# Kernel tuning notes

Hardware: AMD Instinct MI355X
Metric: run time of the kernel (lower is better)

Reference implementation:

```python
import jax, jax.numpy as jnp
import numpy as np

DIM = 256
NUM_HEAD = 8
HEAD_DIM = DIM // NUM_HEAD
SCALE = HEAD_DIM ** -0.5


def setup_inputs() -> dict:
    key = jax.random.key(0)
    ks = jax.random.split(key, 8)
    B, NQ, NK = 8, 512, 4096
    state = jax.random.normal(ks[0], (B, NQ, DIM), dtype=jnp.float32)
    pointcloud = jax.random.normal(ks[1], (B, NK, DIM), dtype=jnp.float32)
    s = 0.02
    Wq = jax.random.normal(ks[2], (DIM, DIM), dtype=jnp.float32) * s
    bq = jnp.zeros((DIM,), dtype=jnp.float32)
    Wkv = jax.random.normal(ks[3], (DIM, 2 * DIM), dtype=jnp.float32) * s
    bkv = jnp.zeros((2 * DIM,), dtype=jnp.float32)
    Wo = jax.random.normal(ks[4], (DIM, DIM), dtype=jnp.float32) * s
    bo = jnp.zeros((DIM,), dtype=jnp.float32)
    return {"state": state, "pointcloud": pointcloud, "Wq": Wq, "bq": bq,
            "Wkv": Wkv, "bkv": bkv, "Wo": Wo, "bo": bo}


def reference(state, pointcloud, Wq, bq, Wkv, bkv, Wo, bo):
    # q: [b, nq, dim]; kv: [b, nk, 2*dim]
    q = state @ Wq + bq
    kv = pointcloud @ Wkv + bkv
    k, v = jnp.split(kv, 2, axis=-1)

    def split_heads(x):
        b, n, _ = x.shape
        return x.reshape(b, n, NUM_HEAD, HEAD_DIM).transpose(0, 2, 1, 3)  # b h n d

    q, k, v = split_heads(q), split_heads(k), split_heads(v)
    attn = jnp.einsum('bhqd,bhkd->bhqk', q, k) * SCALE
    attn = jax.nn.softmax(attn, axis=-1)
    out = jnp.einsum('bhqk,bhkd->bhqd', attn, v)
    b, h, nq, d = out.shape
    out = out.transpose(0, 2, 1, 3).reshape(b, nq, h * d)
    return out @ Wo + bo
```

## Files before the change

### kernel.cpp

```cpp
#include <hip/hip_runtime.h>

typedef unsigned short u16;
typedef unsigned int   u32;
typedef __bf16 bf16x8 __attribute__((ext_vector_type(8)));
typedef float  f32x4  __attribute__((ext_vector_type(4)));
typedef float  f32x16 __attribute__((ext_vector_type(16)));
typedef u32    u32x4  __attribute__((ext_vector_type(4)));
typedef u16    u16x8  __attribute__((ext_vector_type(8)));

#define DEVINL __device__ __forceinline__

DEVINL void glds16(const void* g, void* l) {
  __builtin_amdgcn_global_load_lds((const __attribute__((address_space(1))) u32*)g,
                                   (__attribute__((address_space(3))) u32*)l, 16, 0, 0);
}

DEVINL u16 f2bf(float f) {
  u32 u = __builtin_bit_cast(u32, f);
  u32 r = u + 0x7fffu + ((u >> 16) & 1u);
  return (u16)(r >> 16);
}

DEVINL u32 cvtpk(float lo, float hi) {
  u32 r;
  asm("v_cvt_pk_bf16_f32 %0, %1, %2" : "=v"(r) : "v"(lo), "v"(hi));
  return r;
}

DEVINL u16x8 cvt8(f32x4 a, f32x4 b) {
  u32x4 r = {cvtpk(a[0], a[1]), cvtpk(a[2], a[3]), cvtpk(b[0], b[1]), cvtpk(b[2], b[3])};
  return __builtin_bit_cast(u16x8, r);
}

__global__ __launch_bounds__(256) void prep_k(const float* __restrict__ Wq,
                                              const float* __restrict__ Wkv,
                                              const float* __restrict__ Wo,
                                              const float* __restrict__ state,
                                              const float* __restrict__ pc,
                                              u16* __restrict__ WqT, u16* __restrict__ WkvT,
                                              u16* __restrict__ WoT, u16* __restrict__ sb,
                                              u16* __restrict__ pb) {
  int bid = blockIdx.x, tid = threadIdx.x;
  if (bid < 1024) {
    int i = bid * 256 + tid;
    if (i < 65536) {
      int n = i >> 8, k = i & 255;
      WqT[i] = f2bf(Wq[k * 256 + n]);
    } else if (i < 196608) {
      int j = i - 65536; int n = j >> 8, k = j & 255;
      WkvT[j] = f2bf(Wkv[k * 512 + n]);
    } else {
      int j = i - 196608; int n = j >> 8, k = j & 255;
      WoT[j] = f2bf(Wo[k * 256 + n]);
    }
  } else if (bid < 1536) {
    size_t u = (size_t)(bid - 1024) * 256 + tid;
    f32x4 a = *(const f32x4*)(state + u * 8);
    f32x4 b = *(const f32x4*)(state + u * 8 + 4);
    *(u16x8*)(sb + u * 8) = cvt8(a, b);
  } else {
    size_t u = (size_t)(bid - 1536) * 256 + tid;
    f32x4 a = *(const f32x4*)(pc + u * 8);
    f32x4 b = *(const f32x4*)(pc + u * 8 + 4);
    *(u16x8*)(pb + u * 8) = cvt8(a, b);
  }
}

template<int EPI, bool XCDSWZ>
DEVINL void gemm_body(const u16* __restrict__ A, const u16* __restrict__ Bt,
                      const float* __restrict__ bias, void* __restrict__ Cp,
                      void* __restrict__ C2p, u16* As, u16* Bs,
                      int N, int nmt, float scale, int bid, int nblk) {
  const int K = 256;
  int tid = threadIdx.x, lane = tid & 63, w = tid >> 6;
  int g = lane >> 4, ln15 = lane & 15;
  int mt, nt;
  if (XCDSWZ) {
    int u = (bid & 7) * (nblk >> 3) + (bid >> 3);
    mt = u >> 2; nt = u & 3;
  } else {
    mt = bid % nmt; nt = bid / nmt;
  }
  int arow0 = mt * 128, bcol0 = nt * 128;
  int wr = w >> 1, wc = w & 1;
  f32x4 acc[4][4] = {};

  auto stage = [&](int buf, int kt) {
    #pragma unroll
    for (int i = 0; i < 4; ++i) {
      int c = i * 256 + tid; int row = c >> 3, seg = c & 7;
      glds16(A + (size_t)(arow0 + row) * K + kt * 64 + (seg ^ (row & 7)) * 8,
             (char*)As + (size_t)buf * 16384 + (i * 256 + w * 64) * 16);
      glds16(Bt + (size_t)(bcol0 + row) * K + kt * 64 + (seg ^ (row & 7)) * 8,
             (char*)Bs + (size_t)buf * 16384 + (i * 256 + w * 64) * 16);
    }
  };

  stage(0, 0);
  __syncthreads();
  for (int kt = 0; kt < 4; ++kt) {
    int buf = kt & 1;
    if (kt < 3) stage(buf ^ 1, kt + 1);
    const u16* Ab = As + buf * 8192;
    const u16* Bb = Bs + buf * 8192;
    #pragma unroll
    for (int kk = 0; kk < 2; ++kk) {
      bf16x8 af[4], bfr[4];
      #pragma unroll
      for (int mi = 0; mi < 4; ++mi) {
        int row = wr * 64 + mi * 16 + ln15;
        int idx = row * 8 + ((kk * 4 + g) ^ (row & 7));
        af[mi] = __builtin_bit_cast(bf16x8, *(const u32x4*)&Ab[idx * 8]);
      }
      #pragma unroll
      for (int ni = 0; ni < 4; ++ni) {
        int row = wc * 64 + ni * 16 + ln15;
        int idx = row * 8 + ((kk * 4 + g) ^ (row & 7));
        bfr[ni] = __builtin_bit_cast(bf16x8, *(const u32x4*)&Bb[idx * 8]);
      }
      #pragma unroll
      for (int mi = 0; mi < 4; ++mi)
        #pragma unroll
        for (int ni = 0; ni < 4; ++ni)
          acc[mi][ni] = __builtin_amdgcn_mfma_f32_16x16x32_bf16(af[mi], bfr[ni], acc[mi][ni], 0, 0, 0);
    }
    __syncthreads();
  }
  #pragma unroll
  for (int mi = 0; mi < 4; ++mi) {
    #pragma unroll
    for (int ni = 0; ni < 4; ++ni) {
      int col = bcol0 + wc * 64 + ni * 16 + ln15;
      float bv = bias[col];
      #pragma unroll
      for (int r = 0; r < 4; ++r) {
        int row = arow0 + wr * 64 + mi * 16 + g * 4 + r;
        float v = acc[mi][ni][r] + bv;
        if (EPI == 0) {
          ((float*)Cp)[(size_t)row * N + col] = v;
        } else if (EPI == 1) {
          ((u16*)Cp)[(size_t)row * N + col] = f2bf(v * scale);
        } else {
          int b = row >> 12, nk = row & 4095;
          if (col < 256) {
            int h = col >> 5, d = col & 31;
            ((u16*)Cp)[((size_t)((b << 3) + h) * 4096 + nk) * 32 + d] = f2bf(v);
          } else {
            int c2 = col - 256; int h = c2 >> 5, d = c2 & 31;
            ((u16*)C2p)[((size_t)((b << 3) + h) * 4096 + nk) * 32 + d] = f2bf(v);
          }
        }
      }
    }
  }
}

__global__ __launch_bounds__(256) void gemm12_k(const u16* __restrict__ sb,
                                                const u16* __restrict__ pb,
                                                const u16* __restrict__ WqT,
                                                const u16* __restrict__ WkvT,
                                                const float* __restrict__ bq,
                                                const float* __restrict__ bkv,
                                                u16* __restrict__ qbuf, u16* __restrict__ kbuf,
                                                u16* __restrict__ vbuf, float qscl) {
  __shared__ __align__(16) u16 As[2 * 8192];
  __shared__ __align__(16) u16 Bs[2 * 8192];
  int bid = blockIdx.x;
  if (bid < 1024) {
    gemm_body<2, true >(pb, WkvT, bkv, kbuf, vbuf, As, Bs, 512, 256, 1.f, bid, 1024);
  } else {
    gemm_body<1, false>(sb, WqT, bq, qbuf, nullptr, As, Bs, 256, 32, qscl, bid - 1024, 64);
  }
}

__global__ __launch_bounds__(256) void gemm3_k(const u16* __restrict__ ob,
                                               const u16* __restrict__ WoT,
                                               const float* __restrict__ bo,
                                               float* __restrict__ out) {
  __shared__ __align__(16) u16 As[2 * 8192];
  __shared__ __align__(16) u16 Bs[2 * 8192];
  gemm_body<0, false>(ob, WoT, bo, out, nullptr, As, Bs, 256, 32, 1.f, blockIdx.x, 64);
}

__global__ __launch_bounds__(256) void reduce_k(const float* __restrict__ Op,
                                                const float* __restrict__ Dp,
                                                u16* __restrict__ ob) {
  size_t u = (size_t)blockIdx.x * 256 + threadIdx.x;
  int row = (int)(u >> 5), q8 = (int)(u & 31);
  int h = q8 >> 2;
  size_t base = u * 8;
  f32x4 lo = {}, hi = {};
  float dsum = 0.f;
  #pragma unroll
  for (int ss = 0; ss < 4; ++ss) {
    const float* p = Op + (size_t)ss * 1048576;
    lo += *(const f32x4*)(p + base);
    hi += *(const f32x4*)(p + base + 4);
    dsum += Dp[((size_t)ss * 4096 + row) * 8 + h];
  }
  float inv = 1.0f / dsum;
  lo *= inv; hi *= inv;
  *(u16x8*)(ob + base) = cvt8(lo, hi);
}

__global__ __launch_bounds__(256) void attn_k(const u16* __restrict__ qb,
                                              const u16* __restrict__ kb,
                                              const u16* __restrict__ vb,
                                              float* __restrict__ Op,
                                              float* __restrict__ Dp) {
  __shared__ __align__(16) u16 Ks[2][2048];
  __shared__ __align__(16) u16 Vt[2][2048];
  int tid = threadIdx.x, lane = tid & 63, w = tid >> 6;
  int hi = lane >> 5, ln31 = lane & 31;
  int bid = blockIdx.x;
  int qblk = bid >> 8, r2 = bid & 255, bh = r2 >> 2, s = r2 & 3;
  int b = bh >> 3, h = bh & 7;
  const u16* khead = kb + ((size_t)bh * 4096 + s * 1024) * 32;
  const u16* vhead = vb + ((size_t)bh * 4096 + s * 1024) * 32;
  int qrow0 = b * 512 + qblk * 128 + w * 32;

  bf16x8 qf[2];
  #pragma unroll
  for (int ks = 0; ks < 2; ++ks) {
    const u16* src = qb + (size_t)(qrow0 + ln31) * 256 + h * 32 + ks * 16 + hi * 8;
    qf[ks] = __builtin_bit_cast(bf16x8, *(const u32x4*)src);
  }

  f32x16 O = {};
  float den = 0.f;
  int vrow = tid >> 2, vdc = tid & 3;

  auto loadV = [&](int t) -> u32x4 {
    return *(const u32x4*)(vhead + ((size_t)t * 64 + vrow) * 32 + vdc * 8);
  };
  auto stage = [&](int buf, int t, u32x4 vv) {
    glds16(khead + ((size_t)t * 64 + lane) * 32 + w * 8, (char*)&Ks[buf][0] + w * 1024);
    u16x8 us = __builtin_bit_cast(u16x8, vv);
    #pragma unroll
    for (int j = 0; j < 8; ++j) {
      int d = vdc * 8 + j;
      int cs = (vrow >> 3) ^ j ^ (vdc << 1);
      Vt[buf][d * 64 + cs * 8 + (vrow & 7)] = us[j];
    }
  };

  u32x4 vv = loadV(0);
  stage(0, 0, vv);
  vv = loadV(1);
  __syncthreads();

  for (int t = 0; t < 16; ++t) {
    int buf = t & 1;
    if (t + 1 < 16) {
      stage(buf ^ 1, t + 1, vv);
      vv = loadV(t + 2 < 16 ? t + 2 : 15);
    }
    f32x16 sT[2] = {};
    #pragma unroll
    for (int ks = 0; ks < 2; ++ks) {
      #pragma unroll
      for (int mt = 0; mt < 2; ++mt) {
        const u16* ka = &Ks[buf][((ks * 2 + hi) * 64 + mt * 32 + ln31) * 8];
        bf16x8 kf = __builtin_bit_cast(bf16x8, *(const u32x4*)ka);
        sT[mt] = __builtin_amdgcn_mfma_f32_32x32x16_bf16(kf, qf[ks], sT[mt], 0, 0, 0);
      }
    }
    u32 pa[4][4];
    #pragma unroll
    for (int mt = 0; mt < 2; ++mt) {
      float p[16];
      #pragma unroll
      for (int r = 0; r < 16; ++r) p[r] = __builtin_amdgcn_exp2f(sT[mt][r]);
      #pragma unroll
      for (int r = 0; r < 16; ++r) den += p[r];
      u32 pk0[4], pk1[4];
      #pragma unroll
      for (int c = 0; c < 4; ++c) {
        pk0[c] = cvtpk(p[4*c+0], p[4*c+1]);
        pk1[c] = cvtpk(p[4*c+2], p[4*c+3]);
      }
      u32 a0 = pk0[0], b0 = pk0[1];
      asm("v_permlane32_swap_b32 %0, %1" : "+v"(a0), "+v"(b0));
      u32 a1 = pk1[0], b1 = pk1[1];
      asm("v_permlane32_swap_b32 %0, %1" : "+v"(a1), "+v"(b1));
      u32 a2 = pk0[2], b2 = pk0[3];
      asm("v_permlane32_swap_b32 %0, %1" : "+v"(a2), "+v"(b2));
      u32 a3 = pk1[2], b3 = pk1[3];
      asm("v_permlane32_swap_b32 %0, %1" : "+v"(a3), "+v"(b3));
      pa[mt*2+0][0] = a0; pa[mt*2+0][1] = a1; pa[mt*2+0][2] = b0; pa[mt*2+0][3] = b1;
      pa[mt*2+1][0] = a2; pa[mt*2+1][1] = a3; pa[mt*2+1][2] = b2; pa[mt*2+1][3] = b3;
    }
    #pragma unroll
    for (int kst = 0; kst < 4; ++kst) {
      int cs = (kst * 2 + hi) ^ (ln31 & 7) ^ ((ln31 >> 3) << 1);
      const u16* va = &Vt[buf][ln31 * 64 + cs * 8];
      bf16x8 vf = __builtin_bit_cast(bf16x8, *(const u32x4*)va);
      u32x4 paw = {pa[kst][0], pa[kst][1], pa[kst][2], pa[kst][3]};
      O = __builtin_amdgcn_mfma_f32_32x32x16_bf16(__builtin_bit_cast(bf16x8, paw), vf, O, 0, 0, 0);
    }
    __syncthreads();
  }

  den += __shfl_xor(den, 32);
  float* op = Op + (size_t)s * 1048576;
  #pragma unroll
  for (int r = 0; r < 16; ++r) {
    int qr = 8 * (r >> 2) + 4 * hi + (r & 3);
    op[(size_t)(qrow0 + qr) * 256 + h * 32 + ln31] = O[r];
  }
  if (lane < 32) Dp[(size_t)(s * 4096 + qrow0 + ln31) * 8 + h] = den;
}

extern "C" void kernel_launch(void* const* d_in, const int* in_sizes, int n_in,
                              void* d_out, int out_size, void* d_ws, size_t ws_size,
                              hipStream_t stream) {
  const float* state = (const float*)d_in[0];
  const float* pc    = (const float*)d_in[1];
  const float* Wq    = (const float*)d_in[2];
  const float* bq    = (const float*)d_in[3];
  const float* Wkv   = (const float*)d_in[4];
  const float* bkv   = (const float*)d_in[5];
  const float* Wo    = (const float*)d_in[6];
  const float* bo    = (const float*)d_in[7];
  char* ws = (char*)d_ws;
  u16*   WqT  = (u16*)(ws);
  u16*   WkvT = (u16*)(ws + 131072);
  u16*   WoT  = (u16*)(ws + 393216);
  u16*   sb   = (u16*)(ws + 524288);
  u16*   pb   = (u16*)(ws + 2621440);
  u16*   qb   = (u16*)(ws + 19398656);
  u16*   kb   = (u16*)(ws + 21495808);
  u16*   vb   = (u16*)(ws + 38273024);
  u16*   ob   = (u16*)(ws + 55050240);
  float* Op   = (float*)(ws + 57147392);
  float* Dp   = (float*)(ws + 73924608);

  prep_k<<<5632, 256, 0, stream>>>(Wq, Wkv, Wo, state, pc, WqT, WkvT, WoT, sb, pb);
  const float QSCL = 0.17677669529663687f * 1.4426950408889634f;
  gemm12_k<<<1088, 256, 0, stream>>>(sb, pb, WqT, WkvT, bq, bkv, qb, kb, vb, QSCL);
  attn_k<<<1024, 256, 0, stream>>>(qb, kb, vb, Op, Dp);
  reduce_k<<<512, 256, 0, stream>>>(Op, Dp, ob);
  gemm3_k<<<64, 256, 0, stream>>>(ob, WoT, bo, (float*)d_out);
}
```

Before: 156.8 us.

## Double attention key split to 8 and tile weight transpose via LDS

Attention now splits each head's 4096 keys into 8 chunks instead of 4, doubling the grid to 2048 blocks and halving the per-block key loop, with the reduce kernel summing 8 partials. This targets occupancy and tail effects on a GPU with many CUs. The cost is twice the partial output traffic (the fp32 Op buffer doubles and Dp moves to make room). Separately, the weight transpose-and-convert now uses 64x64 shared-memory tiles with coalesced vector loads and stores instead of strided scalar reads.

```diff
diff --git a/kernel.cpp b/kernel.cpp
--- a/kernel.cpp
+++ b/kernel.cpp
@@ -40,26 +40,37 @@
                                               u16* __restrict__ WqT, u16* __restrict__ WkvT,
                                               u16* __restrict__ WoT, u16* __restrict__ sb,
                                               u16* __restrict__ pb) {
+  __shared__ float Lt[64][65];
   int bid = blockIdx.x, tid = threadIdx.x;
-  if (bid < 1024) {
-    int i = bid * 256 + tid;
-    if (i < 65536) {
-      int n = i >> 8, k = i & 255;
-      WqT[i] = f2bf(Wq[k * 256 + n]);
-    } else if (i < 196608) {
-      int j = i - 65536; int n = j >> 8, k = j & 255;
-      WkvT[j] = f2bf(Wkv[k * 512 + n]);
-    } else {
-      int j = i - 196608; int n = j >> 8, k = j & 255;
-      WoT[j] = f2bf(Wo[k * 256 + n]);
-    }
-  } else if (bid < 1536) {
-    size_t u = (size_t)(bid - 1024) * 256 + tid;
+  if (bid < 64) {
+    const float* W; u16* Wt; int Nw, t;
+    if (bid < 16)      { W = Wq;  Wt = WqT;  Nw = 256; t = bid; }
+    else if (bid < 48) { W = Wkv; Wt = WkvT; Nw = 512; t = bid - 16; }
+    else               { W = Wo;  Wt = WoT;  Nw = 256; t = bid - 48; }
+    int kt0 = (t & 3) * 64, nt0 = (t >> 2) * 64;
+    #pragma unroll
+    for (int i = 0; i < 4; ++i) {
+      int idx = i * 256 + tid;
+      int r = idx >> 4, col = (idx & 15) * 4;
+      f32x4 v = *(const f32x4*)(W + (size_t)(kt0 + r) * Nw + nt0 + col);
+      Lt[r][col] = v[0]; Lt[r][col + 1] = v[1]; Lt[r][col + 2] = v[2]; Lt[r][col + 3] = v[3];
+    }
+    __syncthreads();
+    #pragma unroll
+    for (int j = 0; j < 2; ++j) {
+      int idx = j * 256 + tid;
+      int n = idx >> 3, kc = (idx & 7) * 8;
+      f32x4 a = {Lt[kc + 0][n], Lt[kc + 1][n], Lt[kc + 2][n], Lt[kc + 3][n]};
+      f32x4 b = {Lt[kc + 4][n], Lt[kc + 5][n], Lt[kc + 6][n], Lt[kc + 7][n]};
+      *(u16x8*)(Wt + (size_t)(nt0 + n) * 256 + kt0 + kc) = cvt8(a, b);
+    }
+  } else if (bid < 576) {
+    size_t u = (size_t)(bid - 64) * 256 + tid;
     f32x4 a = *(const f32x4*)(state + u * 8);
     f32x4 b = *(const f32x4*)(state + u * 8 + 4);
     *(u16x8*)(sb + u * 8) = cvt8(a, b);
   } else {
-    size_t u = (size_t)(bid - 1536) * 256 + tid;
+    size_t u = (size_t)(bid - 576) * 256 + tid;
     f32x4 a = *(const f32x4*)(pc + u * 8);
     f32x4 b = *(const f32x4*)(pc + u * 8 + 4);
     *(u16x8*)(pb + u * 8) = cvt8(a, b);
@@ -192,7 +203,7 @@
   f32x4 lo = {}, hi = {};
   float dsum = 0.f;
   #pragma unroll
-  for (int ss = 0; ss < 4; ++ss) {
+  for (int ss = 0; ss < 8; ++ss) {
     const float* p = Op + (size_t)ss * 1048576;
     lo += *(const f32x4*)(p + base);
     hi += *(const f32x4*)(p + base + 4);
@@ -213,10 +224,10 @@
   int tid = threadIdx.x, lane = tid & 63, w = tid >> 6;
   int hi = lane >> 5, ln31 = lane & 31;
   int bid = blockIdx.x;
-  int qblk = bid >> 8, r2 = bid & 255, bh = r2 >> 2, s = r2 & 3;
+  int qblk = bid >> 9, r2 = bid & 511, bh = r2 >> 3, s = r2 & 7;
   int b = bh >> 3, h = bh & 7;
-  const u16* khead = kb + ((size_t)bh * 4096 + s * 1024) * 32;
-  const u16* vhead = vb + ((size_t)bh * 4096 + s * 1024) * 32;
+  const u16* khead = kb + ((size_t)bh * 4096 + s * 512) * 32;
+  const u16* vhead = vb + ((size_t)bh * 4096 + s * 512) * 32;
   int qrow0 = b * 512 + qblk * 128 + w * 32;
 
   bf16x8 qf[2];
@@ -249,11 +260,11 @@
   vv = loadV(1);
   __syncthreads();
 
-  for (int t = 0; t < 16; ++t) {
+  for (int t = 0; t < 8; ++t) {
     int buf = t & 1;
-    if (t + 1 < 16) {
+    if (t + 1 < 8) {
       stage(buf ^ 1, t + 1, vv);
-      vv = loadV(t + 2 < 16 ? t + 2 : 15);
+      vv = loadV(t + 2 < 8 ? t + 2 : 7);
     }
     f32x16 sT[2] = {};
     #pragma unroll
@@ -333,12 +344,12 @@
   u16*   vb   = (u16*)(ws + 38273024);
   u16*   ob   = (u16*)(ws + 55050240);
   float* Op   = (float*)(ws + 57147392);
-  float* Dp   = (float*)(ws + 73924608);
-
-  prep_k<<<5632, 256, 0, stream>>>(Wq, Wkv, Wo, state, pc, WqT, WkvT, WoT, sb, pb);
+  float* Dp   = (float*)(ws + 90701824);
+
+  prep_k<<<4672, 256, 0, stream>>>(Wq, Wkv, Wo, state, pc, WqT, WkvT, WoT, sb, pb);
   const float QSCL = 0.17677669529663687f * 1.4426950408889634f;
   gemm12_k<<<1088, 256, 0, stream>>>(sb, pb, WqT, WkvT, bq, bkv, qb, kb, vb, QSCL);
-  attn_k<<<1024, 256, 0, stream>>>(qb, kb, vb, Op, Dp);
+  attn_k<<<2048, 256, 0, stream>>>(qb, kb, vb, Op, Dp);
   reduce_k<<<512, 256, 0, stream>>>(Op, Dp, ob);
   gemm3_k<<<64, 256, 0, stream>>>(ob, WoT, bo, (float*)d_out);
 }
```

Measured after the change: 158.9 us. About the same (+1.3%).
